# Kernel tuning notes

Measured on AMD Instinct MI355X. Metric: run time of the kernel, lower is better.

The kernel has to match this reference:

```python
import jax, jax.numpy as jnp
import numpy as np

N_NODES = 50000
N_EDGES = 800000
BATCH = 4
D = 64


def setup_inputs() -> dict:
    key = jax.random.key(0)
    ks = jax.random.split(key, 8)
    state = jax.random.normal(ks[0], (BATCH, N_NODES, D), dtype=jnp.float32)
    edge_row = jax.random.randint(ks[1], (N_EDGES,), 0, N_NODES, dtype=jnp.int32)
    edge_col = jax.random.randint(ks[2], (N_EDGES,), 0, N_NODES, dtype=jnp.int32)
    edge_weight = jax.random.uniform(ks[3], (N_EDGES,), dtype=jnp.float32)
    stdv = 1.0 / np.sqrt(D)
    W1 = jax.random.uniform(ks[4], (D, D), minval=-stdv, maxval=stdv, dtype=jnp.float32)
    b1 = jnp.zeros((D,), dtype=jnp.float32)
    W2 = jax.random.uniform(ks[5], (D, D), minval=-stdv, maxval=stdv, dtype=jnp.float32)
    b2 = jnp.zeros((D,), dtype=jnp.float32)
    w_out = jax.random.normal(ks[6], (D,), dtype=jnp.float32) * stdv
    return {"state": state, "edge_row": edge_row, "edge_col": edge_col,
            "edge_weight": edge_weight, "W1": W1, "b1": b1, "W2": W2,
            "b2": b2, "w_out": w_out}


def _gcn_layer(x, W, bias, edge_row, edge_col, edge_weight, n, b):
    # x: [n, b, d_in] -> support [n, b, d_out]
    support = jnp.einsum('nbk,kp->nbp', x, W) + bias
    flat = support.reshape(n, -1)  # [n, b*d_out]
    # sparse spmm: out[i] = sum_{e: row_e=i} w_e * flat[col_e]
    msgs = edge_weight[:, None] * flat[edge_col]  # [E, b*d_out]
    out = jax.ops.segment_sum(msgs, edge_row, num_segments=n)
    return jax.nn.relu(out.reshape(n, b, -1))


def reference(state, edge_row, edge_col, edge_weight, W1, b1, W2, b2, w_out):
    b, n, _ = state.shape
    x = jnp.transpose(state, (1, 0, 2))  # [n, b, d]
    for W, bias in ((W1, b1), (W2, b2)):
        x = _gcn_layer(x, W, bias, edge_row, edge_col, edge_weight, n, b)
    # actor head: Linear(d,1,bias=False), squeeze, transpose -> [b, n]
    logits = jnp.einsum('nbd,d->nb', x, w_out)
    return logits.T
```

## Files before the change

kernel.cpp:

```cpp
#include <hip/hip_runtime.h>


typedef _Float16 fp16_t;
typedef _Float16 h4 __attribute__((ext_vector_type(4)));
typedef _Float16 h8 __attribute__((ext_vector_type(8)));
typedef float    f4 __attribute__((ext_vector_type(4)));
typedef unsigned long long ull;

#define CAP   64
#define RPB   256
#define BCAP  4608
#define CHK   3200
#define LROW  264
#define S1Q   (127.f / 4.f)
#define S1D   (4.f / 127.f)

__global__ __launch_bounds__(256) void b1p_k(const int* __restrict__ erow,
                                             const int* __restrict__ ecol,
                                             const float* __restrict__ ew,
                                             int* __restrict__ gcnt,
                                             ull* __restrict__ bed,
                                             int E, int NB, int NB1,
                                             const float* __restrict__ W,
                                             const float* __restrict__ bias,
                                             fp16_t* __restrict__ wf,
                                             float* __restrict__ bf) {
    if ((int)blockIdx.x == NB1) {
        int lane = threadIdx.x;
        if (lane < 64) {
            int r16 = lane & 15, half = lane >> 4;
#pragma unroll
            for (int kk = 0; kk < 2; ++kk)
#pragma unroll
                for (int j = 0; j < 4; ++j) {
                    h8 v;
#pragma unroll
                    for (int t = 0; t < 8; ++t)
                        v[t] = (_Float16)W[(32 * kk + 8 * half + t) * 64 + 16 * j + r16];
                    *(h8*)&wf[((kk * 4 + j) * 64 + lane) * 8] = v;
                }
#pragma unroll
            for (int j = 0; j < 4; ++j) bf[j * 64 + lane] = bias[16 * j + r16];
        }
        return;
    }
    __shared__ int hist[256], offs[256], cur[256], gbase[256];
    __shared__ ull stage[CHK];
    __shared__ unsigned short sbkt[CHK];
    int tid = threadIdx.x;
    int e0 = blockIdx.x * CHK;
    int e1 = e0 + CHK < E ? e0 + CHK : E;

    hist[tid] = 0;
    cur[tid] = 0;
    __syncthreads();
    for (int e = e0 + tid; e < e1; e += 256)
        atomicAdd(&hist[erow[e] >> 8], 1);
    __syncthreads();
    int v = hist[tid];
    offs[tid] = v;
    __syncthreads();
    for (int off = 1; off < 256; off <<= 1) {
        int t = (tid >= off) ? offs[tid - off] : 0;
        __syncthreads();
        offs[tid] += t;
        __syncthreads();
    }
    offs[tid] -= v;
    if (tid < NB && v > 0) gbase[tid] = atomicAdd(&gcnt[tid], v);
    __syncthreads();
    for (int e = e0 + tid; e < e1; e += 256) {
        int r = erow[e];
        int bk = r >> 8;
        unsigned q = (unsigned)(ew[e] * 32767.f + 0.5f);
        ull pv = ((ull)(r & 255) << 32) | (q << 17) | (unsigned)ecol[e];
        int idx = offs[bk] + atomicAdd(&cur[bk], 1);
        stage[idx] = pv;
        sbkt[idx] = (unsigned short)bk;
    }
    __syncthreads();
    int total = e1 - e0;
    for (int i = tid; i < total; i += 256) {
        int bk = sbkt[i];
        int sl = gbase[bk] + (i - offs[bk]);
        if (sl < BCAP) bed[(size_t)bk * BCAP + sl] = stage[i];
    }
}

__global__ __launch_bounds__(1024) void bg2_k(const ull* __restrict__ bed,
                                              const int* __restrict__ gcnt,
                                              unsigned* __restrict__ ed,
                                              int* __restrict__ cnt,
                                              int N, int NB,
                                              const float* __restrict__ xf,
                                              const float* __restrict__ W,
                                              const float* __restrict__ bias,
                                              unsigned char* __restrict__ flat1) {
    if ((int)blockIdx.x < NB) {
        __shared__ unsigned sbuf[RPB * CAP];
        __shared__ int scnt[RPB];
        int b = blockIdx.x, tid = threadIdx.x;
        for (int i = tid; i < RPB * CAP; i += 1024) sbuf[i] = 0;
        if (tid < RPB) scnt[tid] = 0;
        __syncthreads();
        int n = gcnt[b];
        n = n < BCAP ? n : BCAP;
        const ull* p = bed + (size_t)b * BCAP;
        for (int i = tid; i < n; i += 1024) {
            ull v = p[i];
            int rl = (int)(v >> 32);
            int pos = atomicAdd(&scnt[rl], 1);
            if (pos < CAP) sbuf[(rl << 6) + pos] = (unsigned)v;
        }
        __syncthreads();
        size_t base = (size_t)b * (RPB * CAP);
        for (int i = tid; i < RPB * CAP; i += 1024)
            ed[base + i] = sbuf[i];
        int r = b * RPB + tid;
        if (tid < RPB && r < N) cnt[r] = scnt[tid] < CAP ? scnt[tid] : CAP;
    } else {
        int tid = threadIdx.x;
        int wave = tid >> 6, lane = tid & 63;
        int batch = wave & 3, tsub = wave >> 2;
        int r16 = lane & 15, half = lane >> 4;

        h8 Bf[2][4];
#pragma unroll
        for (int kk = 0; kk < 2; ++kk)
#pragma unroll
            for (int j = 0; j < 4; ++j) {
                h8 v;
#pragma unroll
                for (int t = 0; t < 8; ++t)
                    v[t] = (_Float16)W[(32 * kk + 8 * half + t) * 64 + 16 * j + r16];
                Bf[kk][j] = v;
            }
        float bj[4];
#pragma unroll
        for (int j = 0; j < 4; ++j) bj[j] = bias[16 * j + r16];

        int ntile = N >> 4;
        int gstride = ((int)gridDim.x - NB) * 4;
        for (int tile = ((int)blockIdx.x - NB) * 4 + tsub; tile < ntile;
             tile += gstride) {
            int row = tile * 16 + r16;
            const float* p = xf + ((size_t)batch * N + row) * 64 + 8 * half;
            f4 u0 = *(const f4*)p;
            f4 u1 = *(const f4*)(p + 4);
            f4 u2 = *(const f4*)(p + 32);
            f4 u3 = *(const f4*)(p + 36);
            h8 A0, A1;
#pragma unroll
            for (int t = 0; t < 4; ++t) {
                A0[t] = (_Float16)u0[t]; A0[t + 4] = (_Float16)u1[t];
                A1[t] = (_Float16)u2[t]; A1[t + 4] = (_Float16)u3[t];
            }
#pragma unroll
            for (int j = 0; j < 4; ++j) {
                f4 c = {0.f, 0.f, 0.f, 0.f};
                c = __builtin_amdgcn_mfma_f32_16x16x32_f16(A0, Bf[0][j], c, 0, 0, 0);
                c = __builtin_amdgcn_mfma_f32_16x16x32_f16(A1, Bf[1][j], c, 0, 0, 0);
#pragma unroll
                for (int r = 0; r < 4; ++r) {
                    int orow = tile * 16 + 4 * half + r;
                    float fu = fmaf(c[r] + bj[j], S1Q, 128.f);
                    fu = fminf(fmaxf(fu, 0.f), 255.f);
                    flat1[(size_t)orow * 256 + batch * 64 + 16 * j + r16] =
                        (unsigned char)(fu + 0.5f);
                }
            }
        }
    }
}

#define EDGE4I(pk, A0, A1, A2, A3, WS)                                         \
    {                                                                          \
        unsigned _p = (pk);                                                    \
        float _w = (float)(_p >> 17) * (1.f / 32767.f);                        \
        unsigned _v = *(const unsigned*)(fb + ((size_t)(_p & 0x1FFFFu) << 8)   \
                                         + lane4);                             \
        A0 += _w * (float)(_v & 0xffu);                                        \
        A1 += _w * (float)((_v >> 8) & 0xffu);                                 \
        A2 += _w * (float)((_v >> 16) & 0xffu);                                \
        A3 += _w * (float)(_v >> 24);                                          \
        WS += _w;                                                              \
    }

__global__ __launch_bounds__(256) void spmmG_k(const unsigned char* __restrict__ flat,
                                               const int* __restrict__ cnt,
                                               const unsigned* __restrict__ ed,
                                               const fp16_t* __restrict__ wf,
                                               const float* __restrict__ bf,
                                               unsigned char* __restrict__ flat2i,
                                               float* __restrict__ s2, int N) {
    __shared__ fp16_t sagg[16 * LROW];
    __shared__ h8     swf[8 * 64];
    __shared__ float  sbf[4 * 64];
    int tid  = threadIdx.x;
    int wave = tid >> 6;
    int lane = tid & 63;
    int lane4 = lane * 4;
    int r16 = lane & 15, half = lane >> 4;

    ((f4*)swf)[tid] = ((const f4*)wf)[tid];
    ((f4*)swf)[tid + 256] = ((const f4*)wf)[tid + 256];
    sbf[tid] = bf[tid];

    int blk0 = blockIdx.x * 16;
    const char* fb = (const char*)flat;
    int r0 = blk0 + wave * 4;

    int mm0 = __builtin_amdgcn_readfirstlane(cnt[r0]);
    int mm1 = __builtin_amdgcn_readfirstlane(cnt[r0 + 1]);
    int mm2 = __builtin_amdgcn_readfirstlane(cnt[r0 + 2]);
    int mm3 = __builtin_amdgcn_readfirstlane(cnt[r0 + 3]);
#define C4(a, b) ((((a) > (b) ? (a) : (b)) + 3) & ~3)
    int cA = C4(mm0, mm1) + C4(mm2, mm3);
    int cB = C4(mm0, mm2) + C4(mm1, mm3);
    int cC = C4(mm0, mm3) + C4(mm1, mm2);
    int i1, i2, i3, mI1, mI2, mI3;
    if (cA <= cB && cA <= cC) { i1 = 1; i2 = 2; i3 = 3; mI1 = mm1; mI2 = mm2; mI3 = mm3; }
    else if (cB <= cC)        { i1 = 2; i2 = 1; i3 = 3; mI1 = mm2; mI2 = mm1; mI3 = mm3; }
    else                      { i1 = 3; i2 = 1; i3 = 2; mI1 = mm3; mI2 = mm1; mI3 = mm2; }

    int pa[2] = {0, i2}, pb[2] = {i1, i3};
    int pma[2] = {mm0, mI2}, pmb[2] = {mI1, mI3};
#pragma unroll
    for (int pr = 0; pr < 2; ++pr) {
        int la = pa[pr], lb = pb[pr];
        int mr = C4(pma[pr], pmb[pr]);
        const unsigned* e0 = ed + (size_t)(r0 + la) * CAP;
        const unsigned* e1 = ed + (size_t)(r0 + lb) * CAP;
        float a0 = 0.f, a1 = 0.f, a2 = 0.f, a3 = 0.f, wsA = 0.f;
        float c0 = 0.f, c1 = 0.f, c2 = 0.f, c3 = 0.f, wsC = 0.f;
        for (int j = 0; j < mr; j += 4) {
            uint4 pA = *(const uint4*)(e0 + j);
            uint4 pB = *(const uint4*)(e1 + j);
            EDGE4I(pA.x, a0, a1, a2, a3, wsA) EDGE4I(pB.x, c0, c1, c2, c3, wsC)
            EDGE4I(pA.y, a0, a1, a2, a3, wsA) EDGE4I(pB.y, c0, c1, c2, c3, wsC)
            EDGE4I(pA.z, a0, a1, a2, a3, wsA) EDGE4I(pB.z, c0, c1, c2, c3, wsC)
            EDGE4I(pA.w, a0, a1, a2, a3, wsA) EDGE4I(pB.w, c0, c1, c2, c3, wsC)
        }
        float bA = 128.f * wsA, bC = 128.f * wsC;
        h4 s0, s1;
        s0.x = (fp16_t)fmaxf(S1D * (a0 - bA), 0.f);
        s0.y = (fp16_t)fmaxf(S1D * (a1 - bA), 0.f);
        s0.z = (fp16_t)fmaxf(S1D * (a2 - bA), 0.f);
        s0.w = (fp16_t)fmaxf(S1D * (a3 - bA), 0.f);
        s1.x = (fp16_t)fmaxf(S1D * (c0 - bC), 0.f);
        s1.y = (fp16_t)fmaxf(S1D * (c1 - bC), 0.f);
        s1.z = (fp16_t)fmaxf(S1D * (c2 - bC), 0.f);
        s1.w = (fp16_t)fmaxf(S1D * (c3 - bC), 0.f);
        *(h4*)&sagg[(wave * 4 + la) * LROW + lane4] = s0;
        *(h4*)&sagg[(wave * 4 + lb) * LROW + lane4] = s1;
    }
#undef C4
    __syncthreads();

    h8 A0 = *(const h8*)&sagg[r16 * LROW + wave * 64 + 8 * half];
    h8 A1 = *(const h8*)&sagg[r16 * LROW + wave * 64 + 32 + 8 * half];
    f4 cc[4];
#pragma unroll
    for (int j = 0; j < 4; ++j) {
        f4 c = {0.f, 0.f, 0.f, 0.f};
        c = __builtin_amdgcn_mfma_f32_16x16x32_f16(A0, swf[j * 64 + lane], c, 0, 0, 0);
        c = __builtin_amdgcn_mfma_f32_16x16x32_f16(A1, swf[(4 + j) * 64 + lane], c, 0, 0, 0);
        float bjv = sbf[j * 64 + lane];
        c.x += bjv; c.y += bjv; c.z += bjv; c.w += bjv;
        cc[j] = c;
    }
#pragma unroll
    for (int r = 0; r < 4; ++r) {
        float m = fmaxf(fmaxf(fabsf(cc[0][r]), fabsf(cc[1][r])),
                        fmaxf(fabsf(cc[2][r]), fabsf(cc[3][r])));
        m = fmaxf(m, __shfl_xor(m, 1));
        m = fmaxf(m, __shfl_xor(m, 2));
        m = fmaxf(m, __shfl_xor(m, 4));
        m = fmaxf(m, __shfl_xor(m, 8));
        int orow = blk0 + 4 * half + r;
        float inv = (m > 0.f) ? (127.f / m) : 0.f;
        if (r16 == 0) s2[(orow << 2) | wave] = m * (1.f / 127.f);
#pragma unroll
        for (int j = 0; j < 4; ++j) {
            float q = fmaf(cc[j][r], inv, 128.f);
            flat2i[(size_t)orow * 256 + wave * 64 + 16 * j + r16] =
                (unsigned char)(q + 0.5f);
        }
    }
}

#define EDGE4Q(pk, A0, A1, A2, A3, WS)                                         \
    {                                                                          \
        unsigned _p = (pk);                                                    \
        unsigned _c = _p & 0x1FFFFu;                                           \
        float _w = (float)(_p >> 17) * (1.f / 32767.f) * s2[(_c << 2) | bsel]; \
        unsigned _v = *(const unsigned*)(fb + ((size_t)_c << 8) + lane4);      \
        A0 += _w * (float)(_v & 0xffu);                                        \
        A1 += _w * (float)((_v >> 8) & 0xffu);                                 \
        A2 += _w * (float)((_v >> 16) & 0xffu);                                \
        A3 += _w * (float)(_v >> 24);                                          \
        WS += _w;                                                              \
    }

__global__ __launch_bounds__(256) void spmm2h_k(const unsigned char* __restrict__ flat,
                                                const int* __restrict__ cnt,
                                                const unsigned* __restrict__ ed,
                                                const float* __restrict__ s2,
                                                const float* __restrict__ wout,
                                                float* __restrict__ out, int N) {
    int rowi = blockIdx.x * 4 + (int)(threadIdx.x >> 6);
    int lane = threadIdx.x & 63;
    int lane4 = lane * 4;
    int bsel = lane >> 4;
    const char* fb = (const char*)flat;
    int m = __builtin_amdgcn_readfirstlane(cnt[rowi]);
    int mr = (m + 7) & ~7;
    const unsigned* ep = ed + (size_t)rowi * CAP;
    float a0 = 0.f, a1 = 0.f, a2 = 0.f, a3 = 0.f, ws = 0.f;
    for (int j = 0; j < mr; j += 8) {
        uint4 pA = *(const uint4*)(ep + j);
        uint4 pB = *(const uint4*)(ep + j + 4);
        EDGE4Q(pA.x, a0, a1, a2, a3, ws) EDGE4Q(pA.y, a0, a1, a2, a3, ws)
        EDGE4Q(pA.z, a0, a1, a2, a3, ws) EDGE4Q(pA.w, a0, a1, a2, a3, ws)
        EDGE4Q(pB.x, a0, a1, a2, a3, ws) EDGE4Q(pB.y, a0, a1, a2, a3, ws)
        EDGE4Q(pB.z, a0, a1, a2, a3, ws) EDGE4Q(pB.w, a0, a1, a2, a3, ws)
    }
    float bs = 128.f * ws;
    int t = lane & 15;
    float4 wo = ((const float4*)wout)[t];
    float p = fmaxf(a0 - bs, 0.f) * wo.x + fmaxf(a1 - bs, 0.f) * wo.y +
              fmaxf(a2 - bs, 0.f) * wo.z + fmaxf(a3 - bs, 0.f) * wo.w;
    p += __shfl_xor(p, 1); p += __shfl_xor(p, 2);
    p += __shfl_xor(p, 4); p += __shfl_xor(p, 8);
    if (t == 0) out[(size_t)bsel * N + rowi] = p;
}

extern "C" void kernel_launch(void* const* d_in, const int* in_sizes, int n_in,
                              void* d_out, int out_size, void* d_ws, size_t ws_size,
                              hipStream_t stream) {
    const float* state = (const float*)d_in[0];
    const int*   erow  = (const int*)d_in[1];
    const int*   ecol  = (const int*)d_in[2];
    const float* ew    = (const float*)d_in[3];
    const float* W1    = (const float*)d_in[4];
    const float* b1    = (const float*)d_in[5];
    const float* W2    = (const float*)d_in[6];
    const float* b2    = (const float*)d_in[7];
    const float* wout  = (const float*)d_in[8];
    float* out = (float*)d_out;

    int N = in_sizes[0] / (4 * 64);
    int E = in_sizes[1];
    int NB = (N + RPB - 1) / RPB;

    char* ws = (char*)d_ws;
    size_t off = 0;
    auto alloc = [&](size_t bytes) -> char* {
        char* p = ws + off;
        off += (bytes + 255) & ~(size_t)255;
        return p;
    };
    unsigned char* flat1  = (unsigned char*)alloc((size_t)N * 256);
    unsigned char* flat2i = (unsigned char*)alloc((size_t)N * 256);
    float*    s2    = (float*)alloc((size_t)N * 4 * 4);
    int*      cnt   = (int*)alloc((size_t)NB * RPB * 4);
    unsigned* ed    = (unsigned*)alloc((size_t)NB * RPB * CAP * 4);
    int*      gcnt  = (int*)alloc((size_t)NB * 4);
    ull*      bed   = (ull*)alloc((size_t)NB * BCAP * 8);
    fp16_t*   wf    = (fp16_t*)alloc(8 * 64 * 8 * 2);
    float*    bfr   = (float*)alloc(4 * 64 * 4);
    if (off > ws_size) return;

    int nblk1 = (E + CHK - 1) / CHK;
    hipMemsetAsync(gcnt, 0, (size_t)NB * 4, stream);
    b1p_k<<<nblk1 + 1, 256, 0, stream>>>(erow, ecol, ew, gcnt, bed, E, NB,
                                         nblk1, W2, b2, wf, bfr);
    bg2_k<<<NB + 256, 1024, 0, stream>>>(bed, gcnt, ed, cnt, N, NB,
                                         state, W1, b1, flat1);
    spmmG_k<<<N / 16, 256, 0, stream>>>(flat1, cnt, ed, wf, bfr, flat2i, s2, N);
    spmm2h_k<<<(N + 3) / 4, 256, 0, stream>>>(flat2i, cnt, ed, s2, wout, out, N);
}
```

Measured before the change: 114.1 us.

## Overlap layer-1 GEMM with edge bucketing and split bucket build into own kernel

Moves the dense layer-1 MFMA GEMM from the second-stage build kernel into the first edge-bucketing kernel, so the GEMM runs alongside the histogram/scatter pass instead of alongside the per-bucket compaction. The weight preparation and gcnt zeroing move into a tiny separate kernel, which replaces the memset. The edge chunk size is halved so more bucketing blocks run, and GEMM blocks shrink to 256 threads with 1024 of them. The cost is one extra kernel launch, and more global atomics on gcnt because there are more chunks.

```diff
diff --git a/kernel.cpp b/kernel.cpp
--- a/kernel.cpp
+++ b/kernel.cpp
@@ -10,118 +10,89 @@
 #define CAP   64
 #define RPB   256
 #define BCAP  4608
-#define CHK   3200
+#define CHK   1600
 #define LROW  264
 #define S1Q   (127.f / 4.f)
 #define S1D   (4.f / 127.f)
 
-__global__ __launch_bounds__(256) void b1p_k(const int* __restrict__ erow,
-                                             const int* __restrict__ ecol,
-                                             const float* __restrict__ ew,
-                                             int* __restrict__ gcnt,
-                                             ull* __restrict__ bed,
-                                             int E, int NB, int NB1,
-                                             const float* __restrict__ W,
-                                             const float* __restrict__ bias,
-                                             fp16_t* __restrict__ wf,
-                                             float* __restrict__ bf) {
-    if ((int)blockIdx.x == NB1) {
-        int lane = threadIdx.x;
-        if (lane < 64) {
-            int r16 = lane & 15, half = lane >> 4;
-#pragma unroll
-            for (int kk = 0; kk < 2; ++kk)
-#pragma unroll
-                for (int j = 0; j < 4; ++j) {
-                    h8 v;
-#pragma unroll
-                    for (int t = 0; t < 8; ++t)
-                        v[t] = (_Float16)W[(32 * kk + 8 * half + t) * 64 + 16 * j + r16];
-                    *(h8*)&wf[((kk * 4 + j) * 64 + lane) * 8] = v;
-                }
-#pragma unroll
-            for (int j = 0; j < 4; ++j) bf[j * 64 + lane] = bias[16 * j + r16];
-        }
-        return;
-    }
-    __shared__ int hist[256], offs[256], cur[256], gbase[256];
-    __shared__ ull stage[CHK];
-    __shared__ unsigned short sbkt[CHK];
-    int tid = threadIdx.x;
-    int e0 = blockIdx.x * CHK;
-    int e1 = e0 + CHK < E ? e0 + CHK : E;
-
-    hist[tid] = 0;
-    cur[tid] = 0;
-    __syncthreads();
-    for (int e = e0 + tid; e < e1; e += 256)
-        atomicAdd(&hist[erow[e] >> 8], 1);
-    __syncthreads();
-    int v = hist[tid];
-    offs[tid] = v;
-    __syncthreads();
-    for (int off = 1; off < 256; off <<= 1) {
-        int t = (tid >= off) ? offs[tid - off] : 0;
-        __syncthreads();
-        offs[tid] += t;
-        __syncthreads();
-    }
-    offs[tid] -= v;
-    if (tid < NB && v > 0) gbase[tid] = atomicAdd(&gcnt[tid], v);
-    __syncthreads();
-    for (int e = e0 + tid; e < e1; e += 256) {
-        int r = erow[e];
-        int bk = r >> 8;
-        unsigned q = (unsigned)(ew[e] * 32767.f + 0.5f);
-        ull pv = ((ull)(r & 255) << 32) | (q << 17) | (unsigned)ecol[e];
-        int idx = offs[bk] + atomicAdd(&cur[bk], 1);
-        stage[idx] = pv;
-        sbkt[idx] = (unsigned short)bk;
-    }
-    __syncthreads();
-    int total = e1 - e0;
-    for (int i = tid; i < total; i += 256) {
-        int bk = sbkt[i];
-        int sl = gbase[bk] + (i - offs[bk]);
-        if (sl < BCAP) bed[(size_t)bk * BCAP + sl] = stage[i];
-    }
-}
-
-__global__ __launch_bounds__(1024) void bg2_k(const ull* __restrict__ bed,
-                                              const int* __restrict__ gcnt,
-                                              unsigned* __restrict__ ed,
-                                              int* __restrict__ cnt,
-                                              int N, int NB,
-                                              const float* __restrict__ xf,
-                                              const float* __restrict__ W,
+__global__ __launch_bounds__(64) void prepW_k(const float* __restrict__ W,
                                               const float* __restrict__ bias,
-                                              unsigned char* __restrict__ flat1) {
-    if ((int)blockIdx.x < NB) {
-        __shared__ unsigned sbuf[RPB * CAP];
-        __shared__ int scnt[RPB];
-        int b = blockIdx.x, tid = threadIdx.x;
-        for (int i = tid; i < RPB * CAP; i += 1024) sbuf[i] = 0;
-        if (tid < RPB) scnt[tid] = 0;
-        __syncthreads();
-        int n = gcnt[b];
-        n = n < BCAP ? n : BCAP;
-        const ull* p = bed + (size_t)b * BCAP;
-        for (int i = tid; i < n; i += 1024) {
-            ull v = p[i];
-            int rl = (int)(v >> 32);
-            int pos = atomicAdd(&scnt[rl], 1);
-            if (pos < CAP) sbuf[(rl << 6) + pos] = (unsigned)v;
-        }
-        __syncthreads();
-        size_t base = (size_t)b * (RPB * CAP);
-        for (int i = tid; i < RPB * CAP; i += 1024)
-            ed[base + i] = sbuf[i];
-        int r = b * RPB + tid;
-        if (tid < RPB && r < N) cnt[r] = scnt[tid] < CAP ? scnt[tid] : CAP;
+                                              fp16_t* __restrict__ wf,
+                                              float* __restrict__ bf,
+                                              int* __restrict__ gcnt, int NB) {
+    int lane = threadIdx.x;
+    for (int i = lane; i < NB; i += 64) gcnt[i] = 0;
+    int r16 = lane & 15, half = lane >> 4;
+#pragma unroll
+    for (int kk = 0; kk < 2; ++kk)
+#pragma unroll
+        for (int j = 0; j < 4; ++j) {
+            h8 v;
+#pragma unroll
+            for (int t = 0; t < 8; ++t)
+                v[t] = (_Float16)W[(32 * kk + 8 * half + t) * 64 + 16 * j + r16];
+            *(h8*)&wf[((kk * 4 + j) * 64 + lane) * 8] = v;
+        }
+#pragma unroll
+    for (int j = 0; j < 4; ++j) bf[j * 64 + lane] = bias[16 * j + r16];
+}
+
+__global__ __launch_bounds__(256) void bg_k(const int* __restrict__ erow,
+                                            const int* __restrict__ ecol,
+                                            const float* __restrict__ ew,
+                                            int* __restrict__ gcnt,
+                                            ull* __restrict__ bed,
+                                            int E, int NB, int NB1,
+                                            const float* __restrict__ xf,
+                                            const float* __restrict__ W,
+                                            const float* __restrict__ bias,
+                                            unsigned char* __restrict__ flat1,
+                                            int N) {
+    if ((int)blockIdx.x < NB1) {
+        __shared__ int hist[256], offs[256], cur[256], gbase[256];
+        __shared__ ull stage[CHK];
+        __shared__ unsigned short sbkt[CHK];
+        int tid = threadIdx.x;
+        int e0 = blockIdx.x * CHK;
+        int e1 = e0 + CHK < E ? e0 + CHK : E;
+
+        hist[tid] = 0;
+        cur[tid] = 0;
+        __syncthreads();
+        for (int e = e0 + tid; e < e1; e += 256)
+            atomicAdd(&hist[erow[e] >> 8], 1);
+        __syncthreads();
+        int v = hist[tid];
+        offs[tid] = v;
+        __syncthreads();
+        for (int off = 1; off < 256; off <<= 1) {
+            int t = (tid >= off) ? offs[tid - off] : 0;
+            __syncthreads();
+            offs[tid] += t;
+            __syncthreads();
+        }
+        offs[tid] -= v;
+        if (tid < NB && v > 0) gbase[tid] = atomicAdd(&gcnt[tid], v);
+        __syncthreads();
+        for (int e = e0 + tid; e < e1; e += 256) {
+            int r = erow[e];
+            int bk = r >> 8;
+            unsigned q = (unsigned)(ew[e] * 32767.f + 0.5f);
+            ull pv = ((ull)(r & 255) << 32) | (q << 17) | (unsigned)ecol[e];
+            int idx = offs[bk] + atomicAdd(&cur[bk], 1);
+            stage[idx] = pv;
+            sbkt[idx] = (unsigned short)bk;
+        }
+        __syncthreads();
+        int total = e1 - e0;
+        for (int i = tid; i < total; i += 256) {
+            int bk = sbkt[i];
+            int sl = gbase[bk] + (i - offs[bk]);
+            if (sl < BCAP) bed[(size_t)bk * BCAP + sl] = stage[i];
+        }
     } else {
-        int tid = threadIdx.x;
-        int wave = tid >> 6, lane = tid & 63;
-        int batch = wave & 3, tsub = wave >> 2;
+        int wave = threadIdx.x >> 6;
+        int lane = threadIdx.x & 63;
         int r16 = lane & 15, half = lane >> 4;
 
         h8 Bf[2][4];
@@ -140,11 +111,10 @@
         for (int j = 0; j < 4; ++j) bj[j] = bias[16 * j + r16];
 
         int ntile = N >> 4;
-        int gstride = ((int)gridDim.x - NB) * 4;
-        for (int tile = ((int)blockIdx.x - NB) * 4 + tsub; tile < ntile;
-             tile += gstride) {
+        int gstride = gridDim.x - NB1;
+        for (int tile = blockIdx.x - NB1; tile < ntile; tile += gstride) {
             int row = tile * 16 + r16;
-            const float* p = xf + ((size_t)batch * N + row) * 64 + 8 * half;
+            const float* p = xf + ((size_t)wave * N + row) * 64 + 8 * half;
             f4 u0 = *(const f4*)p;
             f4 u1 = *(const f4*)(p + 4);
             f4 u2 = *(const f4*)(p + 32);
@@ -165,12 +135,39 @@
                     int orow = tile * 16 + 4 * half + r;
                     float fu = fmaf(c[r] + bj[j], S1Q, 128.f);
                     fu = fminf(fmaxf(fu, 0.f), 255.f);
-                    flat1[(size_t)orow * 256 + batch * 64 + 16 * j + r16] =
+                    flat1[(size_t)orow * 256 + wave * 64 + 16 * j + r16] =
                         (unsigned char)(fu + 0.5f);
                 }
             }
         }
     }
+}
+
+__global__ __launch_bounds__(1024) void build2_k(const ull* __restrict__ bed,
+                                                 const int* __restrict__ gcnt,
+                                                 unsigned* __restrict__ ed,
+                                                 int* __restrict__ cnt, int N) {
+    __shared__ unsigned sbuf[RPB * CAP];
+    __shared__ int scnt[RPB];
+    int b = blockIdx.x, tid = threadIdx.x;
+    for (int i = tid; i < RPB * CAP; i += 1024) sbuf[i] = 0;
+    if (tid < RPB) scnt[tid] = 0;
+    __syncthreads();
+    int n = gcnt[b];
+    n = n < BCAP ? n : BCAP;
+    const ull* p = bed + (size_t)b * BCAP;
+    for (int i = tid; i < n; i += 1024) {
+        ull v = p[i];
+        int rl = (int)(v >> 32);
+        int pos = atomicAdd(&scnt[rl], 1);
+        if (pos < CAP) sbuf[(rl << 6) + pos] = (unsigned)v;
+    }
+    __syncthreads();
+    size_t base = (size_t)b * (RPB * CAP);
+    for (int i = tid; i < RPB * CAP; i += 1024)
+        ed[base + i] = sbuf[i];
+    int r = b * RPB + tid;
+    if (tid < RPB && r < N) cnt[r] = scnt[tid] < CAP ? scnt[tid] : CAP;
 }
 
 #define EDGE4I(pk, A0, A1, A2, A3, WS)                                         \
@@ -371,12 +368,11 @@
     float*    bfr   = (float*)alloc(4 * 64 * 4);
     if (off > ws_size) return;
 
+    prepW_k<<<1, 64, 0, stream>>>(W2, b2, wf, bfr, gcnt, NB);
     int nblk1 = (E + CHK - 1) / CHK;
-    hipMemsetAsync(gcnt, 0, (size_t)NB * 4, stream);
-    b1p_k<<<nblk1 + 1, 256, 0, stream>>>(erow, ecol, ew, gcnt, bed, E, NB,
-                                         nblk1, W2, b2, wf, bfr);
-    bg2_k<<<NB + 256, 1024, 0, stream>>>(bed, gcnt, ed, cnt, N, NB,
-                                         state, W1, b1, flat1);
+    bg_k<<<nblk1 + 1024, 256, 0, stream>>>(erow, ecol, ew, gcnt, bed, E, NB,
+                                           nblk1, state, W1, b1, flat1, N);
+    build2_k<<<NB, 1024, 0, stream>>>(bed, gcnt, ed, cnt, N);
     spmmG_k<<<N / 16, 256, 0, stream>>>(flat1, cnt, ed, wf, bfr, flat2i, s2, N);
     spmm2h_k<<<(N + 3) / 4, 256, 0, stream>>>(flat2i, cnt, ed, s2, wout, out, N);
 }
```

New measurement: 113.7 us. About the same (-0.3%).
